# Optimization experiments

Hardware: AMD Instinct MI355X
Metric: run time of the kernel (lower is better)

The kernel has to match this reference:

```python
import jax, jax.numpy as jnp
import numpy as np

B, T, H = 16, 512, 768
S = 32            # gold spans per example
L = 50            # max_span_len -> candidate ends per span
NT = 3            # num_types
HS = 4 * H        # span repr size


def setup_inputs() -> dict:
    key = jax.random.key(0)
    ks = jax.random.split(key, 8)
    h = jax.random.normal(ks[0], (B, T, H), dtype=jnp.float32)
    attention_mask = jnp.ones((B, T), dtype=jnp.int32)
    starts = jax.random.randint(ks[1], (B, S), 1, 400).astype(jnp.int32)
    lens = jax.random.randint(ks[2], (B, S), 0, L).astype(jnp.int32)
    ends = starts + lens                      # <= 448 < last_tok=510
    types = jax.random.randint(ks[3], (B, S), 0, NT).astype(jnp.int32)
    W1 = jax.random.normal(ks[4], (HS, HS), dtype=jnp.float32) * (1.0 / np.sqrt(HS))
    b1 = jnp.zeros((HS,), dtype=jnp.float32)
    w_score = jax.random.normal(ks[5], (HS,), dtype=jnp.float32) * (1.0 / np.sqrt(HS))
    b_score = jnp.zeros((1,), dtype=jnp.float32)
    W_type = jax.random.normal(ks[6], (HS, NT), dtype=jnp.float32) * (1.0 / np.sqrt(HS))
    b_type = jnp.zeros((NT,), dtype=jnp.float32)
    return {"h": h, "attention_mask": attention_mask, "span_starts": starts,
            "span_ends": ends, "span_types": types, "W1": W1, "b1": b1,
            "w_score": w_score, "b_score": b_score, "W_type": W_type, "b_type": b_type}


def _span_loss(h, attention_mask, span_starts, span_ends, span_types,
               W1, b1, w_score, b_score, W_type, b_type, type_loss_weight=1.0):
    cls = h[:, 0]                                              # [B,H]
    # prefix sums for O(1) segment means: pre[b,t] = sum h[b,0:t]
    pre = jnp.concatenate([jnp.zeros((B, 1, H), h.dtype), jnp.cumsum(h, axis=1)], axis=1)

    valid_len = attention_mask.sum(axis=1)                     # [B]
    last_tok = jnp.maximum(1, valid_len - 2)                   # [B]

    s = span_starts                                            # [B,S]
    e_gold = span_ends
    gold_idx = e_gold - s                                      # [B,S]
    lt = last_tok[:, None]
    span_valid = (s >= 1) & (s <= lt) & (e_gold >= s) & (e_gold <= lt) & (gold_idx < L)

    e_max = jnp.minimum(s + L - 1, lt)                         # [B,S]
    p = s[..., None] + jnp.arange(L, dtype=s.dtype)            # [B,S,L] candidate ends
    cand_valid = p <= e_max[..., None]

    sc = jnp.clip(s, 0, T - 1)
    pc = jnp.clip(p, 0, T - 1)
    bi2 = jnp.arange(B)[:, None]
    bi3 = jnp.arange(B)[:, None, None]

    h_start = h[bi2, sc]                                       # [B,S,H]
    h_end = h[bi3, pc]                                         # [B,S,L,H]
    seg_len = jnp.maximum(p - s[..., None] + 1, 1).astype(h.dtype)
    h_mean = (pre[bi3, pc + 1] - pre[bi2, sc][:, :, None]) / seg_len[..., None]

    repr_ = jnp.concatenate([
        jnp.broadcast_to(h_start[:, :, None], (B, S, L, H)),
        h_end,
        h_mean,
        jnp.broadcast_to(cls[:, None, None], (B, S, L, H)),
    ], axis=-1)                                                # [B,S,L,4H]

    h1 = jax.nn.gelu(jnp.einsum('bslh,hd->bsld', repr_, W1) + b1, approximate=False)
    scores = jnp.einsum('bsld,d->bsl', h1, w_score) + b_score[0]      # [B,S,L]
    type_logits = jnp.einsum('bsld,dk->bslk', h1, W_type) + b_type    # [B,S,L,NT]

    # end-index CE over valid candidate ends
    masked = jnp.where(cand_valid, scores, jnp.float32(-1e9))
    logp_end = jax.nn.log_softmax(masked, axis=-1)             # [B,S,L]
    gi = jnp.clip(gold_idx, 0, L - 1)
    end_loss = -jnp.take_along_axis(logp_end, gi[..., None], axis=-1)[..., 0]  # [B,S]

    # type CE at the gold end index
    tl_gold = jnp.take_along_axis(type_logits, gi[..., None, None], axis=2)[:, :, 0]  # [B,S,NT]
    logp_t = jax.nn.log_softmax(tl_gold, axis=-1)
    tg = jnp.clip(span_types, 0, NT - 1)
    type_loss = -jnp.take_along_axis(logp_t, tg[..., None], axis=-1)[..., 0]  # [B,S]

    vmask = span_valid.astype(h.dtype)
    n_seg = vmask.sum()
    denom = jnp.maximum(n_seg, 1.0)
    loss_end = jnp.where(n_seg > 0, (end_loss * vmask).sum() / denom, 0.0)
    loss_type = jnp.where(n_seg > 0, (type_loss * vmask).sum() / denom, 0.0)
    return loss_end + type_loss_weight * loss_type


def reference(h, attention_mask, span_starts, span_ends, span_types,
              W1, b1, w_score, b_score, W_type, b_type):
    return _span_loss(h, attention_mask, span_starts, span_ends, span_types,
                      W1, b1, w_score, b_score, W_type, b_type)
```

## Files before the change

kernel.cpp:

```cpp
#include <hip/hip_runtime.h>
#include <hip/hip_bf16.h>
#include <math.h>

#define B_ 16
#define T_ 512
#define H_ 768
#define S_ 32
#define L_ 50
#define NT_ 3
#define HS_ 3072
#define CH_ 32
#define CT_ 16

#define XROWS 8192
#define YBASE 8192
#define GBASE 16512
#define XYROWS 16400
#define AROWS 17152

typedef __attribute__((ext_vector_type(8))) short short8;
typedef __attribute__((ext_vector_type(16))) float float16v;

__device__ __forceinline__ unsigned short f2bf(float f) {
    __hip_bfloat16 b = __float2bfloat16(f);
    return *(unsigned short*)&b;
}
__device__ __forceinline__ float bf2f(unsigned short u) {
    union { unsigned int i; float f; } v; v.i = ((unsigned int)u) << 16; return v.f;
}
__device__ __forceinline__ void load_lds16(const void* g, void* l) {
    __builtin_amdgcn_global_load_lds((__attribute__((address_space(1))) void*)g,
                                     (__attribute__((address_space(3))) void*)l, 16, 0, 0);
}
__device__ __forceinline__ ushort4 pack4(float4 v) {
    ushort4 o; o.x = f2bf(v.x); o.y = f2bf(v.y); o.z = f2bf(v.z); o.w = f2bf(v.w);
    return o;
}

__device__ __forceinline__ float gelu_exact(float v) {
    float a = fabsf(v) * 0.70710678118654752f;
    float t = __builtin_amdgcn_rcpf(fmaf(a, 0.47047f, 1.0f));
    float poly = t * fmaf(t, fmaf(t, 0.7478556f, -0.0958798f), 0.3480242f);
    float e = __builtin_amdgcn_exp2f(a * a * -1.4426950408889634f);
    float erfa = fmaf(-poly, e, 1.0f);
    float erfv = copysignf(erfa, v);
    return 0.5f * v * (1.0f + erfv);
}

__global__ __launch_bounds__(256) void cumsum_pass1(const float4* __restrict__ h4,
                                                    float4* __restrict__ partial) {
    int idx = blockIdx.x * 256 + threadIdx.x;
    int hd4 = idx % 192; int t = idx / 192; int ch = t % CH_; int b = t / CH_;
    const float4* hp = h4 + ((size_t)b * T_ + ch * CT_) * 192 + hd4;
    float4 acc = {0.f, 0.f, 0.f, 0.f};
#pragma unroll
    for (int tt = 0; tt < CT_; tt++) {
        float4 v = hp[(size_t)tt * 192];
        acc.x += v.x; acc.y += v.y; acc.z += v.z; acc.w += v.w;
    }
    partial[idx] = acc;
}

__global__ __launch_bounds__(256) void cumsum_pass3(const float4* __restrict__ h4,
                                                    const float4* __restrict__ partial,
                                                    ushort4* __restrict__ Ab4) {
    int idx = blockIdx.x * 256 + threadIdx.x;
    int hd4 = idx % 192; int t = idx / 192; int ch = t % CH_; int b = t / CH_;
    float4 acc = {0.f, 0.f, 0.f, 0.f};
#pragma unroll
    for (int c = 0; c < CH_; c++) {
        if (c < ch) {
            float4 v = partial[((size_t)b * CH_ + c) * 192 + hd4];
            acc.x += v.x; acc.y += v.y; acc.z += v.z; acc.w += v.w;
        }
    }
    int row0 = b * T_ + ch * CT_;
    const float4* hp = h4 + (size_t)row0 * 192 + hd4;
    ushort4* hb = Ab4 + (size_t)row0 * 192 + hd4;
    ushort4* pp = Ab4 + ((size_t)(YBASE + b * (T_ + 1) + ch * CT_ + 1)) * 192 + hd4;
    if (ch == 0) {
        ushort4 z = {0, 0, 0, 0};
        Ab4[((size_t)(YBASE + b * (T_ + 1))) * 192 + hd4] = z;
    }
#pragma unroll
    for (int tt = 0; tt < CT_; tt++) {
        float4 hv = hp[(size_t)tt * 192];
        hb[(size_t)tt * 192] = pack4(hv);
        acc.x += hv.x; acc.y += hv.y; acc.z += hv.z; acc.w += hv.w;
        pp[(size_t)tt * 192] = pack4(acc);
    }
}

__global__ void gather_kernel(const float* __restrict__ h,
                              const int* __restrict__ starts,
                              __hip_bfloat16* __restrict__ Ab) {
    int r = blockIdx.x;
    int src_row;
    if (r < B_ * S_) {
        int b = r / S_;
        int sv = starts[r];
        int sc = min(max(sv, 0), T_ - 1);
        src_row = b * T_ + sc;
    } else {
        int b = r - B_ * S_;
        src_row = b * T_;
    }
    __hip_bfloat16* dst = Ab + (size_t)(GBASE + r) * H_;
    for (int j = threadIdx.x; j < H_; j += 256)
        dst[j] = __float2bfloat16(h[(size_t)src_row * H_ + j]);
}

__global__ __launch_bounds__(256) void transpose_w(const float* __restrict__ W1,
                                                   __hip_bfloat16* __restrict__ Wt) {
    __shared__ float tile[64][65];
    int n0 = blockIdx.x * 64, k0 = blockIdx.y * 64;
    int c = threadIdx.x & 63, r0 = threadIdx.x >> 6;
#pragma unroll
    for (int i = 0; i < 16; i++) {
        int r = r0 + i * 4;
        tile[r][c] = W1[(size_t)(k0 + r) * HS_ + n0 + c];
    }
    __syncthreads();
    int p = k0 / H_, kl = k0 % H_;
    __hip_bfloat16* out = Wt + (size_t)p * HS_ * H_;
#pragma unroll
    for (int i = 0; i < 16; i++) {
        int r = r0 + i * 4;
        out[(size_t)(n0 + r) * H_ + kl + c] = __float2bfloat16(tile[c][r]);
    }
}

__global__ __launch_bounds__(256) void mfma_gemm(const __hip_bfloat16* __restrict__ Ab,
                                                 const __hip_bfloat16* __restrict__ Wt,
                                                 __hip_bfloat16* __restrict__ XY,
                                                 float* __restrict__ ST,
                                                 float* __restrict__ CC) {
    constexpr int K = H_;
    __shared__ __hip_bfloat16 As[2 * 128 * 32];
    __shared__ __hip_bfloat16 Bs[2 * 128 * 32];
    int tid = threadIdx.x;
    int wave = tid >> 6, lane = tid & 63;
    int n0 = blockIdx.x * 128, m0 = blockIdx.y * 128;
    int wm = (wave & 1) * 64, wn = (wave >> 1) * 64;

    const __hip_bfloat16* Bt;
    if (m0 < XROWS)            Bt = Wt + (size_t)1 * HS_ * H_;
    else if (m0 < GBASE)       Bt = Wt + (size_t)2 * HS_ * H_;
    else if (m0 < GBASE + 512) Bt = Wt;
    else                       Bt = Wt + (size_t)3 * HS_ * H_;

    float16v acc[2][2] = {};

    int l31 = lane & 31, lh = lane >> 5;

    for (int k0 = 0; k0 < K; k0 += 64) {
        __syncthreads();
#pragma unroll
        for (int i = 0; i < 4; i++) {
            int cid = i * 256 + wave * 64 + lane;
            int hh = cid >> 9, row = (cid >> 2) & 127, pc = cid & 3;
            int lc = pc ^ ((row >> 1) & 3);
            size_t go = (size_t)row * K + k0 + hh * 32 + lc * 8;
            load_lds16(Ab + (size_t)m0 * K + go,
                       (char*)As + (size_t)(i * 256 + wave * 64) * 16);
            load_lds16(Bt + (size_t)n0 * K + go,
                       (char*)Bs + (size_t)(i * 256 + wave * 64) * 16);
        }
        __syncthreads();

        const short* Asp = (const short*)As;
        const short* Bsp = (const short*)Bs;
#pragma unroll
        for (int kk = 0; kk < 4; kk++) {
            int hh = kk >> 1;
            int lc = 2 * (kk & 1) + lh;
            short8 af[2], bf[2];
#pragma unroll
            for (int mi = 0; mi < 2; mi++) {
                int row = wm + mi * 32 + l31;
                int pc = lc ^ ((row >> 1) & 3);
                af[mi] = *(const short8*)&Asp[(hh * 512 + row * 4 + pc) * 8];
            }
#pragma unroll
            for (int ni = 0; ni < 2; ni++) {
                int row = wn + ni * 32 + l31;
                int pc = lc ^ ((row >> 1) & 3);
                bf[ni] = *(const short8*)&Bsp[(hh * 512 + row * 4 + pc) * 8];
            }
#pragma unroll
            for (int mi = 0; mi < 2; mi++)
#pragma unroll
                for (int ni = 0; ni < 2; ni++)
                    acc[mi][ni] = __builtin_amdgcn_mfma_f32_32x32x16_bf16(
                        af[mi], bf[ni], acc[mi][ni], 0, 0, 0);
        }
    }

#pragma unroll
    for (int mi = 0; mi < 2; mi++) {
#pragma unroll
        for (int ni = 0; ni < 2; ni++) {
            int n = n0 + wn + ni * 32 + l31;
#pragma unroll
            for (int r = 0; r < 16; r++) {
                int m = m0 + wm + mi * 32 + (r & 3) + 8 * (r >> 2) + 4 * lh;
                float v = acc[mi][ni][r];
                if (m < XYROWS) {
                    XY[(size_t)m * HS_ + n] = __float2bfloat16(v);
                } else if (m >= GBASE && m < GBASE + 512) {
                    ST[(size_t)(m - GBASE) * HS_ + n] = v;
                } else if (m >= GBASE + 512 && m < GBASE + 528) {
                    CC[(size_t)(m - GBASE - 512) * HS_ + n] = v;
                }
            }
        }
    }
}

__global__ __launch_bounds__(256) void c0_kernel(const float4* __restrict__ ST,
                                                 const float4* __restrict__ CC,
                                                 const float4* __restrict__ b1,
                                                 const float4* __restrict__ w_score,
                                                 ushort4* __restrict__ c0b,
                                                 ushort4* __restrict__ wb16) {
    if (blockIdx.x >= 512 * HS_ / 4 / 256) {
        int i = (blockIdx.x - 512 * HS_ / 4 / 256) * 256 + threadIdx.x;
        wb16[i] = pack4(w_score[i]);
        return;
    }
    int i = blockIdx.x * 256 + threadIdx.x;
    int row = i / (HS_ / 4);
    int b = row >> 5;
    int c4 = i % (HS_ / 4);
    float4 s = ST[i], c = CC[b * (HS_ / 4) + c4], bb = b1[c4];
    float4 v = {s.x + c.x + bb.x, s.y + c.y + bb.y, s.z + c.z + bb.z, s.w + c.w + bb.w};
    c0b[i] = pack4(v);
}

__global__ __launch_bounds__(256) void combine_kernel(
    const unsigned short* __restrict__ c0, const unsigned short* __restrict__ wb16,
    const __hip_bfloat16* __restrict__ XY,
    const float* __restrict__ b_score, const float* __restrict__ W_type,
    const int* __restrict__ starts, const int* __restrict__ ends,
    float* __restrict__ scores, float* __restrict__ tgold) {
    int bs = blockIdx.x;
    int b = bs >> 5;
    int wave = threadIdx.x >> 6, lane = threadIdx.x & 63;
    int pr = blockIdx.y * 4 + wave;
    if (pr >= L_ / 2) return;
    int l0 = pr * 2, l1 = l0 + 1;
    int sv = starts[bs], ev = ends[bs];
    int gi = min(max(ev - sv, 0), L_ - 1);
    int sc = min(max(sv, 0), T_ - 1);
    int pc0 = min(max(sv + l0, 0), T_ - 1);
    int pc1 = min(max(sv + l1, 0), T_ - 1);
    float inv0 = 1.0f / (float)(l0 + 1);
    float inv1 = 1.0f / (float)(l1 + 1);
    bool isg0 = (l0 == gi), isg1 = (l1 == gi);
    bool anyg = isg0 || isg1;

    const unsigned short* X0 = (const unsigned short*)(XY + (size_t)(b * T_ + pc0) * HS_);
    const unsigned short* X1 = (const unsigned short*)(XY + (size_t)(b * T_ + pc1) * HS_);
    const unsigned short* Y0 = (const unsigned short*)(XY + (size_t)(YBASE + b * (T_ + 1) + pc0 + 1) * HS_);
    const unsigned short* Y1 = (const unsigned short*)(XY + (size_t)(YBASE + b * (T_ + 1) + pc1 + 1) * HS_);
    const unsigned short* Ysr = (const unsigned short*)(XY + (size_t)(YBASE + b * (T_ + 1) + sc) * HS_);
    const unsigned short* c0r = c0 + (size_t)bs * HS_;

    float local0 = 0.f, local1 = 0.f, t0 = 0.f, t1 = 0.f, t2 = 0.f;
#pragma unroll
    for (int j = 0; j < 6; j++) {
        int d = j * 512 + lane * 8;
        short8 xv0 = *(const short8*)(X0 + d);
        short8 xv1 = *(const short8*)(X1 + d);
        short8 yv0 = *(const short8*)(Y0 + d);
        short8 yv1 = *(const short8*)(Y1 + d);
        short8 sv8 = *(const short8*)(Ysr + d);
        short8 cv8 = *(const short8*)(c0r + d);
        short8 wv8 = *(const short8*)(wb16 + d);
#pragma unroll
        for (int q = 0; q < 8; q++) {
            float ys = bf2f(((const unsigned short*)&sv8)[q]);
            float cv = bf2f(((const unsigned short*)&cv8)[q]);
            float w  = bf2f(((const unsigned short*)&wv8)[q]);
            float v0 = fmaf(bf2f(((const unsigned short*)&yv0)[q]) - ys, inv0, cv) +
                       bf2f(((const unsigned short*)&xv0)[q]);
            float v1 = fmaf(bf2f(((const unsigned short*)&yv1)[q]) - ys, inv1, cv) +
                       bf2f(((const unsigned short*)&xv1)[q]);
            float g0 = gelu_exact(v0);
            float g1 = gelu_exact(v1);
            local0 = fmaf(g0, w, local0);
            local1 = fmaf(g1, w, local1);
            if (anyg) {
                float gg = isg0 ? g0 : g1;
                t0 = fmaf(gg, W_type[(d + q) * NT_ + 0], t0);
                t1 = fmaf(gg, W_type[(d + q) * NT_ + 1], t1);
                t2 = fmaf(gg, W_type[(d + q) * NT_ + 2], t2);
            }
        }
    }
#pragma unroll
    for (int off = 32; off >= 1; off >>= 1) {
        local0 += __shfl_down(local0, off);
        local1 += __shfl_down(local1, off);
    }
    if (lane == 0) {
        float bs0 = b_score[0];
        scores[(size_t)bs * L_ + l0] = local0 + bs0;
        scores[(size_t)bs * L_ + l1] = local1 + bs0;
    }
    if (anyg) {
#pragma unroll
        for (int off = 32; off >= 1; off >>= 1) {
            t0 += __shfl_down(t0, off);
            t1 += __shfl_down(t1, off);
            t2 += __shfl_down(t2, off);
        }
        if (lane == 0) {
            tgold[bs * NT_ + 0] = t0;
            tgold[bs * NT_ + 1] = t1;
            tgold[bs * NT_ + 2] = t2;
        }
    }
}

__global__ __launch_bounds__(512) void loss_kernel(
    const float* __restrict__ scores, const float* __restrict__ tgold,
    const int* __restrict__ mask, const int* __restrict__ starts,
    const int* __restrict__ ends, const int* __restrict__ types,
    const float* __restrict__ b_type, float* __restrict__ out) {
    __shared__ int svl[B_];
    __shared__ float r[3][8];
    int tid = threadIdx.x;
    int b = tid / S_;
    if (tid < B_) svl[tid] = 0;
    __syncthreads();
    {
        int part = 0;
        const int* mp = mask + tid * 16;
#pragma unroll
        for (int i = 0; i < 16; i++) part += mp[i];
        atomicAdd(&svl[tid / (T_ / 16)], part);
    }
    __syncthreads();
    int vl = svl[b];
    int lt = max(1, vl - 2);
    int sv = starts[tid], ev = ends[tid];
    int gold = ev - sv;
    bool valid = (sv >= 1) && (sv <= lt) && (ev >= sv) && (ev <= lt) && (gold < L_);
    int emax = min(sv + L_ - 1, lt);
    const float* sp = scores + (size_t)tid * L_;
    float m = -1e30f;
    for (int l = 0; l < L_; l++) {
        float v = (sv + l <= emax) ? sp[l] : -1e9f;
        m = fmaxf(m, v);
    }
    float sum = 0.f;
    for (int l = 0; l < L_; l++) {
        float v = (sv + l <= emax) ? sp[l] : -1e9f;
        sum += expf(v - m);
    }
    int gi = min(max(gold, 0), L_ - 1);
    float vg = (sv + gi <= emax) ? sp[gi] : -1e9f;
    float end_loss = (m + logf(sum)) - vg;

    float t0 = tgold[tid * 3 + 0] + b_type[0];
    float t1 = tgold[tid * 3 + 1] + b_type[1];
    float t2 = tgold[tid * 3 + 2] + b_type[2];
    float tm = fmaxf(t0, fmaxf(t1, t2));
    float tsum = expf(t0 - tm) + expf(t1 - tm) + expf(t2 - tm);
    int tg = min(max(types[tid], 0), NT_ - 1);
    float tv = (tg == 0) ? t0 : ((tg == 1) ? t1 : t2);
    float type_loss = (tm + logf(tsum)) - tv;

    float ve = valid ? end_loss : 0.f;
    float vt = valid ? type_loss : 0.f;
    float vc = valid ? 1.f : 0.f;
    for (int off = 32; off >= 1; off >>= 1) {
        ve += __shfl_down(ve, off);
        vt += __shfl_down(vt, off);
        vc += __shfl_down(vc, off);
    }
    if ((tid & 63) == 0) {
        int w = tid >> 6;
        r[0][w] = ve; r[1][w] = vt; r[2][w] = vc;
    }
    __syncthreads();
    if (tid == 0) {
        float se = 0, st = 0, n = 0;
        for (int w = 0; w < 8; w++) { se += r[0][w]; st += r[1][w]; n += r[2][w]; }
        float denom = fmaxf(n, 1.f);
        out[0] = (n > 0.f) ? (se / denom + st / denom) : 0.f;
    }
}

extern "C" void kernel_launch(void* const* d_in, const int* in_sizes, int n_in,
                              void* d_out, int out_size, void* d_ws, size_t ws_size,
                              hipStream_t stream) {
    const float* h       = (const float*)d_in[0];
    const int*   mask    = (const int*)d_in[1];
    const int*   starts  = (const int*)d_in[2];
    const int*   ends    = (const int*)d_in[3];
    const int*   types   = (const int*)d_in[4];
    const float* W1      = (const float*)d_in[5];
    const float* b1      = (const float*)d_in[6];
    const float* w_score = (const float*)d_in[7];
    const float* b_score = (const float*)d_in[8];
    const float* W_type  = (const float*)d_in[9];
    const float* b_type  = (const float*)d_in[10];
    float* out = (float*)d_out;

    char* ws = (char*)d_ws;
    size_t off = 0;
    __hip_bfloat16* Ab = (__hip_bfloat16*)(ws + off); off += (size_t)AROWS * H_ * 2;
    __hip_bfloat16* XY = (__hip_bfloat16*)(ws + off); off += (size_t)XYROWS * HS_ * 2;
    __hip_bfloat16* Wt = (__hip_bfloat16*)(ws + off); off += (size_t)4 * HS_ * H_ * 2;
    float* ST     = (float*)(ws + off);               off += (size_t)512 * HS_ * 4;
    float* CC     = (float*)(ws + off);               off += (size_t)16 * HS_ * 4;
    unsigned short* c0b = (unsigned short*)(ws + off); off += (size_t)512 * HS_ * 2;
    unsigned short* wb16 = (unsigned short*)(ws + off); off += (size_t)HS_ * 2;
    float* scores = (float*)(ws + off);               off += (size_t)B_ * S_ * L_ * 4;
    float* tgold  = (float*)(ws + off);               off += (size_t)B_ * S_ * NT_ * 4;
    float4* partial = (float4*)XY;

    hipLaunchKernelGGL(cumsum_pass1, dim3(B_ * CH_ * 192 / 256), dim3(256), 0, stream,
                       (const float4*)h, partial);
    hipLaunchKernelGGL(cumsum_pass3, dim3(B_ * CH_ * 192 / 256), dim3(256), 0, stream,
                       (const float4*)h, partial, (ushort4*)Ab);
    hipLaunchKernelGGL(gather_kernel, dim3(B_ * S_ + B_), dim3(256), 0, stream, h, starts, Ab);
    hipLaunchKernelGGL(transpose_w, dim3(48, 48), dim3(256), 0, stream, W1, Wt);

    hipLaunchKernelGGL(mfma_gemm, dim3(24, AROWS / 128), dim3(256), 0, stream,
                       Ab, Wt, XY, ST, CC);
    hipLaunchKernelGGL(c0_kernel, dim3(512 * HS_ / 4 / 256 + 3), dim3(256), 0, stream,
                       (const float4*)ST, (const float4*)CC, (const float4*)b1,
                       (const float4*)w_score, (ushort4*)c0b, (ushort4*)wb16);
    hipLaunchKernelGGL(combine_kernel, dim3(B_ * S_, 7), dim3(256), 0, stream,
                       c0b, wb16, XY, b_score, W_type, starts, ends, scores, tgold);
    hipLaunchKernelGGL(loss_kernel, dim3(1), dim3(512), 0, stream,
                       scores, tgold, mask, starts, ends, types, b_type, out);
}
```

Baseline: 332.0 us.

## Merge prep kernels and fuse bias/CLS add into GEMM epilogue

Merges cumsum pass1, the W1 transpose, the start-row gather and the w_score conversion into one block-partitioned prep kernel. The CLS-row projection (16 rows) moves from the MFMA GEMM to a scalar FP32 dot product inside the prep kernel. The GEMM epilogue now adds that CLS term and b1 and writes bf16 c0 directly, which removes the ST buffer and the separate c0 kernel. This cuts three launches and an FP32 intermediate round trip. In exchange, the scalar CLS loop over strided W1 columns may be slow and could lengthen the prep kernel's tail.

```diff
diff --git a/kernel.cpp b/kernel.cpp
--- a/kernel.cpp
+++ b/kernel.cpp
@@ -17,6 +17,12 @@
 #define GBASE 16512
 #define XYROWS 16400
 #define AROWS 17152
+#define PB_CUM 384
+#define PB_TRW 2304
+#define PB_GAT 512
+#define PB_CC  192
+#define PB_WB  3
+#define PREP_BLOCKS (PB_CUM + PB_TRW + PB_GAT + PB_CC + PB_WB)
 
 typedef __attribute__((ext_vector_type(8))) short short8;
 typedef __attribute__((ext_vector_type(16))) float float16v;
@@ -47,18 +53,70 @@
     return 0.5f * v * (1.0f + erfv);
 }
 
-__global__ __launch_bounds__(256) void cumsum_pass1(const float4* __restrict__ h4,
-                                                    float4* __restrict__ partial) {
-    int idx = blockIdx.x * 256 + threadIdx.x;
-    int hd4 = idx % 192; int t = idx / 192; int ch = t % CH_; int b = t / CH_;
-    const float4* hp = h4 + ((size_t)b * T_ + ch * CT_) * 192 + hd4;
-    float4 acc = {0.f, 0.f, 0.f, 0.f};
-#pragma unroll
-    for (int tt = 0; tt < CT_; tt++) {
-        float4 v = hp[(size_t)tt * 192];
-        acc.x += v.x; acc.y += v.y; acc.z += v.z; acc.w += v.w;
-    }
-    partial[idx] = acc;
+__global__ __launch_bounds__(256) void prep_kernel(
+    const float4* __restrict__ h4, const float* __restrict__ h,
+    const int* __restrict__ starts, const float* __restrict__ W1,
+    const float4* __restrict__ w_score,
+    float4* __restrict__ partial, __hip_bfloat16* __restrict__ Ab,
+    __hip_bfloat16* __restrict__ Wt, float* __restrict__ CC,
+    ushort4* __restrict__ wb16) {
+    __shared__ float tile[64][65];
+    int bx = blockIdx.x, tid = threadIdx.x;
+
+    if (bx < PB_CUM) {
+        int idx = bx * 256 + tid;
+        int hd4 = idx % 192; int t = idx / 192; int ch = t % CH_; int b = t / CH_;
+        const float4* hp = h4 + ((size_t)b * T_ + ch * CT_) * 192 + hd4;
+        float4 acc = {0.f, 0.f, 0.f, 0.f};
+#pragma unroll
+        for (int tt = 0; tt < CT_; tt++) {
+            float4 v = hp[(size_t)tt * 192];
+            acc.x += v.x; acc.y += v.y; acc.z += v.z; acc.w += v.w;
+        }
+        partial[idx] = acc;
+    } else if (bx < PB_CUM + PB_TRW) {
+        int q = bx - PB_CUM;
+        int n0 = (q % 48) * 64, k0 = (q / 48) * 64;
+        int c = tid & 63, r0 = tid >> 6;
+#pragma unroll
+        for (int i = 0; i < 16; i++) {
+            int r = r0 + i * 4;
+            tile[r][c] = W1[(size_t)(k0 + r) * HS_ + n0 + c];
+        }
+        __syncthreads();
+        int p = k0 / H_, kl = k0 % H_;
+        __hip_bfloat16* out = Wt + (size_t)p * HS_ * H_;
+#pragma unroll
+        for (int i = 0; i < 16; i++) {
+            int r = r0 + i * 4;
+            out[(size_t)(n0 + r) * H_ + kl + c] = __float2bfloat16(tile[c][r]);
+        }
+    } else if (bx < PB_CUM + PB_TRW + PB_GAT) {
+        int r = bx - (PB_CUM + PB_TRW);
+        int b = r / S_;
+        int sv = starts[r];
+        int sc = min(max(sv, 0), T_ - 1);
+        const float* src = h + (size_t)(b * T_ + sc) * H_;
+        __hip_bfloat16* dst = Ab + (size_t)(GBASE + r) * H_;
+        for (int j = tid; j < H_; j += 256)
+            dst[j] = __float2bfloat16(src[j]);
+    } else if (bx < PB_CUM + PB_TRW + PB_GAT + PB_CC) {
+        int q = bx - (PB_CUM + PB_TRW + PB_GAT);
+        int b = q / 12, n0 = (q % 12) * 256;
+        float* hs = &tile[0][0];
+        const float* hrow = h + (size_t)b * T_ * H_;
+        for (int j = tid; j < H_; j += 256) hs[j] = hrow[j];
+        __syncthreads();
+        int d = n0 + tid;
+        const float* wp = W1 + (size_t)2304 * HS_ + d;
+        float acc = 0.f;
+#pragma unroll 8
+        for (int k = 0; k < H_; k++) acc = fmaf(hs[k], wp[(size_t)k * HS_], acc);
+        CC[(size_t)b * HS_ + d] = acc;
+    } else {
+        int i = (bx - (PB_CUM + PB_TRW + PB_GAT + PB_CC)) * 256 + tid;
+        wb16[i] = pack4(w_score[i]);
+    }
 }
 
 __global__ __launch_bounds__(256) void cumsum_pass3(const float4* __restrict__ h4,
@@ -91,50 +149,12 @@
     }
 }
 
-__global__ void gather_kernel(const float* __restrict__ h,
-                              const int* __restrict__ starts,
-                              __hip_bfloat16* __restrict__ Ab) {
-    int r = blockIdx.x;
-    int src_row;
-    if (r < B_ * S_) {
-        int b = r / S_;
-        int sv = starts[r];
-        int sc = min(max(sv, 0), T_ - 1);
-        src_row = b * T_ + sc;
-    } else {
-        int b = r - B_ * S_;
-        src_row = b * T_;
-    }
-    __hip_bfloat16* dst = Ab + (size_t)(GBASE + r) * H_;
-    for (int j = threadIdx.x; j < H_; j += 256)
-        dst[j] = __float2bfloat16(h[(size_t)src_row * H_ + j]);
-}
-
-__global__ __launch_bounds__(256) void transpose_w(const float* __restrict__ W1,
-                                                   __hip_bfloat16* __restrict__ Wt) {
-    __shared__ float tile[64][65];
-    int n0 = blockIdx.x * 64, k0 = blockIdx.y * 64;
-    int c = threadIdx.x & 63, r0 = threadIdx.x >> 6;
-#pragma unroll
-    for (int i = 0; i < 16; i++) {
-        int r = r0 + i * 4;
-        tile[r][c] = W1[(size_t)(k0 + r) * HS_ + n0 + c];
-    }
-    __syncthreads();
-    int p = k0 / H_, kl = k0 % H_;
-    __hip_bfloat16* out = Wt + (size_t)p * HS_ * H_;
-#pragma unroll
-    for (int i = 0; i < 16; i++) {
-        int r = r0 + i * 4;
-        out[(size_t)(n0 + r) * H_ + kl + c] = __float2bfloat16(tile[c][r]);
-    }
-}
-
 __global__ __launch_bounds__(256) void mfma_gemm(const __hip_bfloat16* __restrict__ Ab,
                                                  const __hip_bfloat16* __restrict__ Wt,
+                                                 const float* __restrict__ CC,
+                                                 const float* __restrict__ b1,
                                                  __hip_bfloat16* __restrict__ XY,
-                                                 float* __restrict__ ST,
-                                                 float* __restrict__ CC) {
+                                                 unsigned short* __restrict__ c0b) {
     constexpr int K = H_;
     __shared__ __hip_bfloat16 As[2 * 128 * 32];
     __shared__ __hip_bfloat16 Bs[2 * 128 * 32];
@@ -146,8 +166,7 @@
     const __hip_bfloat16* Bt;
     if (m0 < XROWS)            Bt = Wt + (size_t)1 * HS_ * H_;
     else if (m0 < GBASE)       Bt = Wt + (size_t)2 * HS_ * H_;
-    else if (m0 < GBASE + 512) Bt = Wt;
-    else                       Bt = Wt + (size_t)3 * HS_ * H_;
+    else                       Bt = Wt;
 
     float16v acc[2][2] = {};
 
@@ -207,34 +226,15 @@
                 float v = acc[mi][ni][r];
                 if (m < XYROWS) {
                     XY[(size_t)m * HS_ + n] = __float2bfloat16(v);
-                } else if (m >= GBASE && m < GBASE + 512) {
-                    ST[(size_t)(m - GBASE) * HS_ + n] = v;
-                } else if (m >= GBASE + 512 && m < GBASE + 528) {
-                    CC[(size_t)(m - GBASE - 512) * HS_ + n] = v;
+                } else if (m >= GBASE) {
+                    int bsI = m - GBASE;
+                    int bb = bsI >> 5;
+                    c0b[(size_t)bsI * HS_ + n] =
+                        f2bf(v + CC[(size_t)bb * HS_ + n] + b1[n]);
                 }
             }
         }
     }
-}
-
-__global__ __launch_bounds__(256) void c0_kernel(const float4* __restrict__ ST,
-                                                 const float4* __restrict__ CC,
-                                                 const float4* __restrict__ b1,
-                                                 const float4* __restrict__ w_score,
-                                                 ushort4* __restrict__ c0b,
-                                                 ushort4* __restrict__ wb16) {
-    if (blockIdx.x >= 512 * HS_ / 4 / 256) {
-        int i = (blockIdx.x - 512 * HS_ / 4 / 256) * 256 + threadIdx.x;
-        wb16[i] = pack4(w_score[i]);
-        return;
-    }
-    int i = blockIdx.x * 256 + threadIdx.x;
-    int row = i / (HS_ / 4);
-    int b = row >> 5;
-    int c4 = i % (HS_ / 4);
-    float4 s = ST[i], c = CC[b * (HS_ / 4) + c4], bb = b1[c4];
-    float4 v = {s.x + c.x + bb.x, s.y + c.y + bb.y, s.z + c.z + bb.z, s.w + c.w + bb.w};
-    c0b[i] = pack4(v);
 }
 
 __global__ __launch_bounds__(256) void combine_kernel(
@@ -414,7 +414,6 @@
     __hip_bfloat16* Ab = (__hip_bfloat16*)(ws + off); off += (size_t)AROWS * H_ * 2;
     __hip_bfloat16* XY = (__hip_bfloat16*)(ws + off); off += (size_t)XYROWS * HS_ * 2;
     __hip_bfloat16* Wt = (__hip_bfloat16*)(ws + off); off += (size_t)4 * HS_ * H_ * 2;
-    float* ST     = (float*)(ws + off);               off += (size_t)512 * HS_ * 4;
     float* CC     = (float*)(ws + off);               off += (size_t)16 * HS_ * 4;
     unsigned short* c0b = (unsigned short*)(ws + off); off += (size_t)512 * HS_ * 2;
     unsigned short* wb16 = (unsigned short*)(ws + off); off += (size_t)HS_ * 2;
@@ -422,18 +421,13 @@
     float* tgold  = (float*)(ws + off);               off += (size_t)B_ * S_ * NT_ * 4;
     float4* partial = (float4*)XY;
 
-    hipLaunchKernelGGL(cumsum_pass1, dim3(B_ * CH_ * 192 / 256), dim3(256), 0, stream,
-                       (const float4*)h, partial);
+    hipLaunchKernelGGL(prep_kernel, dim3(PREP_BLOCKS), dim3(256), 0, stream,
+                       (const float4*)h, h, starts, W1, (const float4*)w_score,
+                       partial, Ab, Wt, CC, (ushort4*)wb16);
     hipLaunchKernelGGL(cumsum_pass3, dim3(B_ * CH_ * 192 / 256), dim3(256), 0, stream,
-                       (const float4*)h, partial, (ushort4*)Ab);
-    hipLaunchKernelGGL(gather_kernel, dim3(B_ * S_ + B_), dim3(256), 0, stream, h, starts, Ab);
-    hipLaunchKernelGGL(transpose_w, dim3(48, 48), dim3(256), 0, stream, W1, Wt);
-
-    hipLaunchKernelGGL(mfma_gemm, dim3(24, AROWS / 128), dim3(256), 0, stream,
-                       Ab, Wt, XY, ST, CC);
-    hipLaunchKernelGGL(c0_kernel, dim3(512 * HS_ / 4 / 256 + 3), dim3(256), 0, stream,
-                       (const float4*)ST, (const float4*)CC, (const float4*)b1,
-                       (const float4*)w_score, (ushort4*)c0b, (ushort4*)wb16);
+                       (const float4*)h, (const float4*)partial, (ushort4*)Ab);
+    hipLaunchKernelGGL(mfma_gemm, dim3(24, (GBASE + 512) / 128), dim3(256), 0, stream,
+                       Ab, Wt, CC, b1, XY, c0b);
     hipLaunchKernelGGL(combine_kernel, dim3(B_ * S_, 7), dim3(256), 0, stream,
                        c0b, wb16, XY, b_score, W_type, starts, ends, scores, tgold);
     hipLaunchKernelGGL(loss_kernel, dim3(1), dim3(512), 0, stream,
```

Result: slower. 363.7 us (+9.6%).
